# Performance work log

Measured on AMD Instinct MI355X. Metric: run time of the kernel, lower is better.

Reference implementation:

```python
import jax, jax.numpy as jnp
import numpy as np

DIM = 1024
NUM_HEADS = 16
HEAD_DIM = DIM // NUM_HEADS
B, S = 2, 2048


def setup_inputs() -> dict:
    key = jax.random.key(0)
    ks = jax.random.split(key, 7)
    x = jax.random.normal(ks[0], (B, S, DIM), dtype=jnp.float32)
    cos = jax.random.uniform(ks[1], (S, HEAD_DIM // 2), dtype=jnp.float32)
    sin = jax.random.uniform(ks[2], (S, HEAD_DIM // 2), dtype=jnp.float32)
    scale = 1.0 / np.sqrt(DIM)
    Wq = jax.random.normal(ks[3], (DIM, DIM), dtype=jnp.float32) * scale
    Wk = jax.random.normal(ks[4], (DIM, DIM), dtype=jnp.float32) * scale
    Wv = jax.random.normal(ks[5], (DIM, DIM), dtype=jnp.float32) * scale
    Wo = jax.random.normal(ks[6], (DIM, DIM), dtype=jnp.float32) * scale
    return {"x": x, "cos": cos, "sin": sin, "Wq": Wq, "Wk": Wk, "Wv": Wv, "Wo": Wo}


def _apply_rope(t, c, s):
    # t: [B, S, H, hd]; c, s: [1, S, 1, hd] (already doubled)
    half = t.shape[-1] // 2
    t1, t2 = t[..., :half], t[..., half:]
    rot = jnp.concatenate([-t2, t1], axis=-1)
    return t * c + rot * s


def reference(x, cos, sin, Wq, Wk, Wv, Wo):
    Bs, Ss, D = x.shape
    H, hd = NUM_HEADS, HEAD_DIM
    q = (x @ Wq).reshape(Bs, Ss, H, hd)
    k = (x @ Wk).reshape(Bs, Ss, H, hd)
    v = (x @ Wv).reshape(Bs, Ss, H, hd)
    # repeat(1,1,1,2) in torch tiles cos as [cos, cos] along last dim
    c = jnp.concatenate([cos, cos], axis=-1)[None, :, None, :]
    s = jnp.concatenate([sin, sin], axis=-1)[None, :, None, :]
    q = _apply_rope(q, c, s)
    k = _apply_rope(k, c, s)
    # SDPA, non-causal, scale 1/sqrt(hd)
    scores = jnp.einsum("bqhd,bkhd->bhqk", q, k) / jnp.sqrt(jnp.float32(hd))
    attn = jax.nn.softmax(scores, axis=-1)
    out = jnp.einsum("bhqk,bkhd->bqhd", attn, v).reshape(Bs, Ss, D)
    return out @ Wo
```

## Files before the change

kernel.cpp:

```cpp
#include <hip/hip_runtime.h>

#define B_  2
#define S_  2048
#define D_  1024
#define H_  16
#define HD_ 64
#define M_  (B_*S_)

typedef __bf16 bf16x8 __attribute__((ext_vector_type(8)));
typedef float  f32x4  __attribute__((ext_vector_type(4)));
typedef float  f32x16 __attribute__((ext_vector_type(16)));
typedef unsigned short ushort_t;

static __device__ __forceinline__ ushort_t f2bf(float f) {
  __bf16 b = (__bf16)f;
  return __builtin_bit_cast(ushort_t, b);
}
static __device__ __forceinline__ float bf2f(ushort_t u) {
  return (float)__builtin_bit_cast(__bf16, u);
}

typedef __attribute__((address_space(1))) const unsigned u32g;
typedef __attribute__((address_space(3))) unsigned u32l;
static __device__ __forceinline__ void gll16(const ushort_t* g, __bf16* l) {
  __builtin_amdgcn_global_load_lds((u32g*)g, (u32l*)l, 16, 0, 0);
}

__global__ __launch_bounds__(256) void convert_x(const float* __restrict__ x,
                                                 ushort_t* __restrict__ xb) {
  size_t e = ((size_t)blockIdx.x * 256 + threadIdx.x) * 8;
  float4 a = *(const float4*)(x + e);
  float4 b = *(const float4*)(x + e + 4);
  uint4 pk;
  pk.x = (unsigned)f2bf(a.x) | ((unsigned)f2bf(a.y) << 16);
  pk.y = (unsigned)f2bf(a.z) | ((unsigned)f2bf(a.w) << 16);
  pk.z = (unsigned)f2bf(b.x) | ((unsigned)f2bf(b.y) << 16);
  pk.w = (unsigned)f2bf(b.z) | ((unsigned)f2bf(b.w) << 16);
  *(uint4*)(xb + e) = pk;
}

__global__ __launch_bounds__(256) void transpose_w(const float* __restrict__ Wq,
                                                   const float* __restrict__ Wk,
                                                   const float* __restrict__ Wv,
                                                   const float* __restrict__ Wo,
                                                   ushort_t* __restrict__ Wqkvt,
                                                   ushort_t* __restrict__ Wot) {
  __shared__ __bf16 T[64][72];
  const int z = blockIdx.z;
  const float* W = (z == 0) ? Wq : (z == 1) ? Wk : (z == 2) ? Wv : Wo;
  ushort_t* Wt = (z < 3) ? (Wqkvt + (size_t)z * 1048576) : Wot;
  const int k0 = blockIdx.y * 64, n0 = blockIdx.x * 64;
  const int t = threadIdx.x, r = t >> 2, c16 = (t & 3) * 16;
#pragma unroll
  for (int i = 0; i < 4; i++) {
    float4 v = *(const float4*)(W + (size_t)(k0 + r) * D_ + n0 + c16 + i * 4);
    T[r][c16 + i*4 + 0] = (__bf16)v.x;
    T[r][c16 + i*4 + 1] = (__bf16)v.y;
    T[r][c16 + i*4 + 2] = (__bf16)v.z;
    T[r][c16 + i*4 + 3] = (__bf16)v.w;
  }
  __syncthreads();
  ushort_t vals[16];
#pragma unroll
  for (int i = 0; i < 16; i++) vals[i] = __builtin_bit_cast(ushort_t, T[c16 + i][r]);
  ushort_t* dst = Wt + (size_t)(n0 + r) * D_ + k0 + c16;
  *(uint4*)dst       = *(const uint4*)&vals[0];
  *(uint4*)(dst + 8) = *(const uint4*)&vals[8];
}

__global__ __launch_bounds__(256) void transpose_v(const ushort_t* __restrict__ Vb,
                                                   ushort_t* __restrict__ Vtg) {
  __shared__ __bf16 T[64][72];
  const int bh = blockIdx.y, kt = blockIdx.x;
  const int t = threadIdx.x, r = t >> 2, c16 = (t & 3) * 16;
  const ushort_t* src = Vb + ((size_t)bh * S_ + kt*64 + r) * 64 + c16;
  *(uint4*)&T[r][c16]     = *(const uint4*)src;
  *(uint4*)&T[r][c16 + 8] = *(const uint4*)(src + 8);
  __syncthreads();
  ushort_t vals[16];
#pragma unroll
  for (int i = 0; i < 16; i++) {
    int c = c16 + i;
    int k = ((c & 1) << 5) | (c >> 1);
    vals[i] = __builtin_bit_cast(ushort_t, T[k][r]);
  }
  ushort_t* dst = Vtg + ((size_t)bh * 64 + r) * S_ + kt*64 + c16;
  *(uint4*)dst       = *(const uint4*)&vals[0];
  *(uint4*)(dst + 8) = *(const uint4*)&vals[8];
}

template<int OMODE, int BN>
__global__ __launch_bounds__(256) void gemm_bf16(const ushort_t* __restrict__ A,
                                                 const ushort_t* __restrict__ Bt,
                                                 void* __restrict__ Cp,
                                                 const float* __restrict__ cosb,
                                                 const float* __restrict__ sinb) {
  constexpr int NF = BN / 32;
  __shared__ __bf16 As[4096];
  __shared__ __bf16 Bs[BN * 32];
  const int t = threadIdx.x, w = t >> 6, lane = t & 63, l15 = lane & 15, g = lane >> 4;
  const int wr = w >> 1, wc = w & 1;
  const int row0 = blockIdx.y * 128, col0 = blockIdx.x * BN;
  const int lr = t >> 2, lc = (t & 3) * 8;
  f32x4 acc[4][NF] = {};

  for (int k0 = 0; k0 < D_; k0 += 32) {
    __syncthreads();
#pragma unroll
    for (int i = 0; i < 2; i++)
      gll16(A + (size_t)(row0 + i*64 + lr) * D_ + k0 + lc, &As[i*2048 + w*512]);
#pragma unroll
    for (int i = 0; i < BN/64; i++)
      gll16(Bt + (size_t)(col0 + i*64 + lr) * D_ + k0 + lc, &Bs[i*2048 + w*512]);
    __syncthreads();
    bf16x8 af[4], bfv[NF];
#pragma unroll
    for (int mt = 0; mt < 4; mt++)  af[mt]  = *(const bf16x8*)&As[(wr*64 + mt*16 + l15)*32 + g*8];
#pragma unroll
    for (int nt = 0; nt < NF; nt++) bfv[nt] = *(const bf16x8*)&Bs[(wc*(BN/2) + nt*16 + l15)*32 + g*8];
#pragma unroll
    for (int mt = 0; mt < 4; mt++)
#pragma unroll
      for (int nt = 0; nt < NF; nt++)
        acc[mt][nt] = __builtin_amdgcn_mfma_f32_16x16x32_bf16(af[mt], bfv[nt], acc[mt][nt], 0, 0, 0);
  }

  if (OMODE == 0) {
#pragma unroll
    for (int mt = 0; mt < 4; mt++)
#pragma unroll
      for (int nt = 0; nt < NF; nt++) {
        int col = col0 + wc*(BN/2) + nt*16 + l15;
#pragma unroll
        for (int reg = 0; reg < 4; reg++) {
          int r = row0 + wr*64 + mt*16 + g*4 + reg;
          ((float*)Cp)[(size_t)r * D_ + col] = acc[mt][nt][reg];
        }
      }
  } else {
    const int mat = col0 >> 10;
    const int nc0 = (col0 + wc*64) & 1023;
    const int h = nc0 >> 6;
    ushort_t* dst = (ushort_t*)Cp + (size_t)mat * 4194304;
    const float QS = 0.125f * 1.4426950408889634f;
#pragma unroll
    for (int mt = 0; mt < 4; mt++) {
#pragma unroll
      for (int reg = 0; reg < 4; reg++) {
        int r = row0 + wr*64 + mt*16 + g*4 + reg;
        int b = r >> 11, s = r & (S_ - 1);
        size_t base = (((size_t)(b*H_ + h) * S_ + s) << 6);
        if (mat < 2) {
#pragma unroll
          for (int nt = 0; nt < 2; nt++) {
            int d1 = nt*16 + l15;
            float c  = cosb[s*32 + d1];
            float sn = sinb[s*32 + d1];
            float v1 = acc[mt][nt][reg], v2 = acc[mt][nt+2][reg];
            float r1 = v1*c - v2*sn;
            float r2 = v2*c + v1*sn;
            if (mat == 0) { r1 *= QS; r2 *= QS; }
            dst[base + d1]      = f2bf(r1);
            dst[base + d1 + 32] = f2bf(r2);
          }
        } else {
#pragma unroll
          for (int nt = 0; nt < 4; nt++)
            dst[base + nt*16 + l15] = f2bf(acc[mt][nt][reg]);
        }
      }
    }
  }
}

__global__ __launch_bounds__(256) void attn32(const ushort_t* __restrict__ Q,
                                              const ushort_t* __restrict__ K,
                                              const ushort_t* __restrict__ Vtg,
                                              ushort_t* __restrict__ op0,
                                              ushort_t* __restrict__ op1,
                                              float* __restrict__ lw) {
  __shared__ __bf16 KsL[128 * 64];
  __shared__ __bf16 VtL[64 * 128];
  __shared__ __bf16 Ps[4][32][72];
  const int t = threadIdx.x, w = t >> 6, lane = t & 63;
  const int l31 = lane & 31, h2 = lane >> 5, sw = l31 & 7;
  const int bh = blockIdx.y, q0 = blockIdx.x * 128 + w * 32, z = blockIdx.z;

  const ushort_t* Qp = Q + ((size_t)bh * S_ + q0 + l31) * HD_;
  bf16x8 qf[4];
#pragma unroll
  for (int kc = 0; kc < 4; kc++) qf[kc] = *(const bf16x8*)(Qp + kc*16 + h2*8);

  f32x16 o0 = {}, o1 = {};
  float lp[16];
#pragma unroll
  for (int i = 0; i < 16; i++) lp[i] = 0.f;

  const ushort_t* Kb = K   + ((size_t)bh * S_ + z * 1024) * HD_;
  const ushort_t* Vg = Vtg + (size_t)bh * HD_ * S_ + z * 1024;

  const int krl = lane >> 3;
  const int kco = ((lane & 7) ^ krl) * 8;
  const int vrl = lane >> 4;

  for (int kt = 0; kt < 8; kt++) {
    __syncthreads();
#pragma unroll
    for (int p = 0; p < 4; p++) {
      int bk = w*8 + p*32;
      gll16(Kb + (size_t)(kt*128 + bk + krl) * HD_ + kco, &KsL[(bk)*64]);
    }
#pragma unroll
    for (int p = 0; p < 4; p++) {
      int bd = w*4 + p*16;
      int d  = bd + vrl;
      int cd = (lane & 8) | ((lane & 7) ^ (d & 7));
      gll16(Vg + (size_t)d * S_ + kt*128 + cd*8, &VtL[(bd)*128]);
    }
    __syncthreads();

#pragma unroll
    for (int ph = 0; ph < 2; ph++) {
      f32x16 s0 = {}, s1 = {};
#pragma unroll
      for (int kc = 0; kc < 4; kc++) {
        int c = kc*2 + h2;
        int cs = (c ^ sw) * 8;
        bf16x8 b0 = *(const bf16x8*)&KsL[(ph*64 + l31)*64      + cs];
        bf16x8 b1 = *(const bf16x8*)&KsL[(ph*64 + 32 + l31)*64 + cs];
        s0 = __builtin_amdgcn_mfma_f32_32x32x16_bf16(qf[kc], b0, s0, 0, 0, 0);
        s1 = __builtin_amdgcn_mfma_f32_32x32x16_bf16(qf[kc], b1, s1, 0, 0, 0);
      }

#pragma unroll
      for (int i = 0; i < 16; i++) {
        float p0 = __builtin_amdgcn_exp2f(s0[i]);
        float p1 = __builtin_amdgcn_exp2f(s1[i]);
        lp[i] += p0 + p1;
        int row = (i & 3) + 8*(i >> 2) + 4*h2;
        unsigned pk = (unsigned)f2bf(p0) | ((unsigned)f2bf(p1) << 16);
        *(unsigned*)&Ps[w][row][2*l31] = pk;
      }

#pragma unroll
      for (int kc = 0; kc < 4; kc++) {
        int c = kc*2 + h2;
        int cs = (ph*8 | (c ^ sw)) * 8;
        bf16x8 pf = *(const bf16x8*)&Ps[w][l31][kc*16 + h2*8];
        bf16x8 v0 = *(const bf16x8*)&VtL[(l31)*128      + cs];
        bf16x8 v1 = *(const bf16x8*)&VtL[(32 + l31)*128 + cs];
        o0 = __builtin_amdgcn_mfma_f32_32x32x16_bf16(pf, v0, o0, 0, 0, 0);
        o1 = __builtin_amdgcn_mfma_f32_32x32x16_bf16(pf, v1, o1, 0, 0, 0);
      }
    }
  }

#pragma unroll
  for (int i = 0; i < 16; i++) {
#pragma unroll
    for (int mk = 1; mk < 32; mk <<= 1) lp[i] += __shfl_xor(lp[i], mk, 64);
  }

  ushort_t* op = (z == 0) ? op0 : op1;
  float* lwp = lw + (size_t)(z*32 + bh) * S_;
#pragma unroll
  for (int i = 0; i < 16; i++) {
    int row = q0 + (i & 3) + 8*(i >> 2) + 4*h2;
    size_t base = ((size_t)bh * S_ + row) * 64;
    op[base + l31]      = f2bf(o0[i]);
    op[base + 32 + l31] = f2bf(o1[i]);
    if (l31 == 0) lwp[row] = lp[i];
  }
}

__global__ __launch_bounds__(256) void combine(const ushort_t* __restrict__ op0,
                                               const ushort_t* __restrict__ op1,
                                               const float* __restrict__ lw,
                                               ushort_t* __restrict__ att) {
  int tid = blockIdx.x * 256 + threadIdx.x;
  int d8 = (tid & 7) * 8;
  int s  = (tid >> 3) & (S_ - 1);
  int bh = tid >> 14;
  size_t pb = ((size_t)bh * S_ + s) * 64 + d8;
  uint4 a = *(const uint4*)(op0 + pb);
  uint4 b = *(const uint4*)(op1 + pb);
  float inv = 1.f / (lw[(size_t)bh * S_ + s] + lw[(size_t)(32 + bh) * S_ + s]);
  const ushort_t* as = (const ushort_t*)&a;
  const ushort_t* bs = (const ushort_t*)&b;
  ushort_t outv[8];
#pragma unroll
  for (int i = 0; i < 8; i++)
    outv[i] = f2bf((bf2f(as[i]) + bf2f(bs[i])) * inv);
  int bidx = bh >> 4, h = bh & 15;
  *(uint4*)(att + ((size_t)(bidx * S_ + s)) * D_ + h*64 + d8) = *(const uint4*)outv;
}

extern "C" void kernel_launch(void* const* d_in, const int* in_sizes, int n_in,
                              void* d_out, int out_size, void* d_ws, size_t ws_size,
                              hipStream_t stream) {
  (void)in_sizes; (void)n_in; (void)out_size; (void)ws_size;
  const float* x    = (const float*)d_in[0];
  const float* cosb = (const float*)d_in[1];
  const float* sinb = (const float*)d_in[2];
  const float* Wq   = (const float*)d_in[3];
  const float* Wk   = (const float*)d_in[4];
  const float* Wv   = (const float*)d_in[5];
  const float* Wo   = (const float*)d_in[6];
  float* out = (float*)d_out;

  ushort_t* w     = (ushort_t*)d_ws;
  ushort_t* xb    = w;
  ushort_t* Wqkvt = w + 4194304;
  ushort_t* Wot   = w + 7340032;
  ushort_t* Qb    = w + 8388608;
  ushort_t* Kb    = w + 12582912;
  ushort_t* Vb    = w + 16777216;
  ushort_t* Vtg   = w + 20971520;
  ushort_t* att   = w + 25165824;
  float*    lw    = (float*)Wqkvt;

  convert_x<<<2048, 256, 0, stream>>>(x, xb);
  transpose_w<<<dim3(16, 16, 4), 256, 0, stream>>>(Wq, Wk, Wv, Wo, Wqkvt, Wot);

  gemm_bf16<1,128><<<dim3(24, 32), 256, 0, stream>>>(xb, Wqkvt, Qb, cosb, sinb);

  transpose_v<<<dim3(32, 32), 256, 0, stream>>>(Vb, Vtg);

  attn32<<<dim3(16, 32, 2), 256, 0, stream>>>(Qb, Kb, Vtg, xb, Vb, lw);

  combine<<<2048, 256, 0, stream>>>(xb, Vb, lw, att);

  gemm_bf16<0,64><<<dim3(16, 32), 256, 0, stream>>>(att, Wot, out, nullptr, nullptr);
}
```

Baseline: 214.5 us.

## Merge input conversion kernels and XOR-swizzle attention P tile in LDS

Combines the x fp32-to-bf16 conversion and the weight transpose into one prep launch, selected by block index, which removes one kernel launch and its tail. In the attention kernel the padded per-wave P staging buffer is replaced by an unpadded 64-column layout with XOR swizzling on 8-element chunks, so the packed writes and the bf16x8 reads avoid LDS bank conflicts. The swizzle also shrinks LDS usage slightly. The block-index branch in prep gives the two halves different per-thread work within one grid.

```diff
diff --git a/kernel.cpp b/kernel.cpp
--- a/kernel.cpp
+++ b/kernel.cpp
@@ -26,31 +26,34 @@
   __builtin_amdgcn_global_load_lds((u32g*)g, (u32l*)l, 16, 0, 0);
 }
 
-__global__ __launch_bounds__(256) void convert_x(const float* __restrict__ x,
-                                                 ushort_t* __restrict__ xb) {
-  size_t e = ((size_t)blockIdx.x * 256 + threadIdx.x) * 8;
-  float4 a = *(const float4*)(x + e);
-  float4 b = *(const float4*)(x + e + 4);
-  uint4 pk;
-  pk.x = (unsigned)f2bf(a.x) | ((unsigned)f2bf(a.y) << 16);
-  pk.y = (unsigned)f2bf(a.z) | ((unsigned)f2bf(a.w) << 16);
-  pk.z = (unsigned)f2bf(b.x) | ((unsigned)f2bf(b.y) << 16);
-  pk.w = (unsigned)f2bf(b.z) | ((unsigned)f2bf(b.w) << 16);
-  *(uint4*)(xb + e) = pk;
-}
-
-__global__ __launch_bounds__(256) void transpose_w(const float* __restrict__ Wq,
-                                                   const float* __restrict__ Wk,
-                                                   const float* __restrict__ Wv,
-                                                   const float* __restrict__ Wo,
-                                                   ushort_t* __restrict__ Wqkvt,
-                                                   ushort_t* __restrict__ Wot) {
+__global__ __launch_bounds__(256) void prep(const float* __restrict__ x,
+                                            ushort_t* __restrict__ xb,
+                                            const float* __restrict__ Wq,
+                                            const float* __restrict__ Wk,
+                                            const float* __restrict__ Wv,
+                                            const float* __restrict__ Wo,
+                                            ushort_t* __restrict__ Wqkvt,
+                                            ushort_t* __restrict__ Wot) {
   __shared__ __bf16 T[64][72];
-  const int z = blockIdx.z;
+  const int id = blockIdx.x, t = threadIdx.x;
+  if (id < 2048) {
+    size_t e = ((size_t)id * 256 + t) * 8;
+    float4 a = *(const float4*)(x + e);
+    float4 b = *(const float4*)(x + e + 4);
+    uint4 pk;
+    pk.x = (unsigned)f2bf(a.x) | ((unsigned)f2bf(a.y) << 16);
+    pk.y = (unsigned)f2bf(a.z) | ((unsigned)f2bf(a.w) << 16);
+    pk.z = (unsigned)f2bf(b.x) | ((unsigned)f2bf(b.y) << 16);
+    pk.w = (unsigned)f2bf(b.z) | ((unsigned)f2bf(b.w) << 16);
+    *(uint4*)(xb + e) = pk;
+    return;
+  }
+  const int wid = id - 2048;
+  const int z = wid >> 8, ky = (wid >> 4) & 15, nx = wid & 15;
   const float* W = (z == 0) ? Wq : (z == 1) ? Wk : (z == 2) ? Wv : Wo;
   ushort_t* Wt = (z < 3) ? (Wqkvt + (size_t)z * 1048576) : Wot;
-  const int k0 = blockIdx.y * 64, n0 = blockIdx.x * 64;
-  const int t = threadIdx.x, r = t >> 2, c16 = (t & 3) * 16;
+  const int k0 = ky * 64, n0 = nx * 64;
+  const int r = t >> 2, c16 = (t & 3) * 16;
 #pragma unroll
   for (int i = 0; i < 4; i++) {
     float4 v = *(const float4*)(W + (size_t)(k0 + r) * D_ + n0 + c16 + i * 4);
@@ -181,7 +184,7 @@
                                               float* __restrict__ lw) {
   __shared__ __bf16 KsL[128 * 64];
   __shared__ __bf16 VtL[64 * 128];
-  __shared__ __bf16 Ps[4][32][72];
+  __shared__ __bf16 Ps[4][32 * 64];
   const int t = threadIdx.x, w = t >> 6, lane = t & 63;
   const int l31 = lane & 31, h2 = lane >> 5, sw = l31 & 7;
   const int bh = blockIdx.y, q0 = blockIdx.x * 128 + w * 32, z = blockIdx.z;
@@ -198,7 +201,6 @@
 
   const ushort_t* Kb = K   + ((size_t)bh * S_ + z * 1024) * HD_;
   const ushort_t* Vg = Vtg + (size_t)bh * HD_ * S_ + z * 1024;
-
   const int krl = lane >> 3;
   const int kco = ((lane & 7) ^ krl) * 8;
   const int vrl = lane >> 4;
@@ -208,14 +210,14 @@
 #pragma unroll
     for (int p = 0; p < 4; p++) {
       int bk = w*8 + p*32;
-      gll16(Kb + (size_t)(kt*128 + bk + krl) * HD_ + kco, &KsL[(bk)*64]);
+      gll16(Kb + (size_t)(kt*128 + bk + krl) * HD_ + kco, &KsL[bk*64]);
     }
 #pragma unroll
     for (int p = 0; p < 4; p++) {
       int bd = w*4 + p*16;
       int d  = bd + vrl;
       int cd = (lane & 8) | ((lane & 7) ^ (d & 7));
-      gll16(Vg + (size_t)d * S_ + kt*128 + cd*8, &VtL[(bd)*128]);
+      gll16(Vg + (size_t)d * S_ + kt*128 + cd*8, &VtL[bd*128]);
     }
     __syncthreads();
 
@@ -224,8 +226,7 @@
       f32x16 s0 = {}, s1 = {};
 #pragma unroll
       for (int kc = 0; kc < 4; kc++) {
-        int c = kc*2 + h2;
-        int cs = (c ^ sw) * 8;
+        int cs = ((kc*2 + h2) ^ sw) * 8;
         bf16x8 b0 = *(const bf16x8*)&KsL[(ph*64 + l31)*64      + cs];
         bf16x8 b1 = *(const bf16x8*)&KsL[(ph*64 + 32 + l31)*64 + cs];
         s0 = __builtin_amdgcn_mfma_f32_32x32x16_bf16(qf[kc], b0, s0, 0, 0, 0);
@@ -239,16 +240,15 @@
         lp[i] += p0 + p1;
         int row = (i & 3) + 8*(i >> 2) + 4*h2;
         unsigned pk = (unsigned)f2bf(p0) | ((unsigned)f2bf(p1) << 16);
-        *(unsigned*)&Ps[w][row][2*l31] = pk;
+        *(unsigned*)&Ps[w][row*64 + ((l31 >> 2) ^ (row & 7))*8 + (l31 & 3)*2] = pk;
       }
 
 #pragma unroll
       for (int kc = 0; kc < 4; kc++) {
-        int c = kc*2 + h2;
-        int cs = (ph*8 | (c ^ sw)) * 8;
-        bf16x8 pf = *(const bf16x8*)&Ps[w][l31][kc*16 + h2*8];
-        bf16x8 v0 = *(const bf16x8*)&VtL[(l31)*128      + cs];
-        bf16x8 v1 = *(const bf16x8*)&VtL[(32 + l31)*128 + cs];
+        int cs = ((kc*2 + h2) ^ sw) * 8;
+        bf16x8 pf = *(const bf16x8*)&Ps[w][l31*64 + cs];
+        bf16x8 v0 = *(const bf16x8*)&VtL[l31*128      + (ph*8 | ((kc*2 + h2) ^ sw))*8];
+        bf16x8 v1 = *(const bf16x8*)&VtL[(32 + l31)*128 + (ph*8 | ((kc*2 + h2) ^ sw))*8];
         o0 = __builtin_amdgcn_mfma_f32_32x32x16_bf16(pf, v0, o0, 0, 0, 0);
         o1 = __builtin_amdgcn_mfma_f32_32x32x16_bf16(pf, v1, o1, 0, 0, 0);
       }
@@ -319,8 +319,7 @@
   ushort_t* att   = w + 25165824;
   float*    lw    = (float*)Wqkvt;
 
-  convert_x<<<2048, 256, 0, stream>>>(x, xb);
-  transpose_w<<<dim3(16, 16, 4), 256, 0, stream>>>(Wq, Wk, Wv, Wo, Wqkvt, Wot);
+  prep<<<3072, 256, 0, stream>>>(x, xb, Wq, Wk, Wv, Wo, Wqkvt, Wot);
 
   gemm_bf16<1,128><<<dim3(24, 32), 256, 0, stream>>>(xb, Wqkvt, Qb, cosb, sinb);
 
```

Result: no change. 213.3 us (-0.6%).
